# Optimization experiments

Measured on AMD Instinct MI355X. Metric: run time of the kernel, lower is better.

The kernel has to match this reference:

```python
import jax, jax.numpy as jnp
import numpy as np

RANK = 16
ALPHA = 32
SCALING = ALPHA / RANK  # alpha / rank


def setup_inputs() -> dict:
    key = jax.random.key(0)
    k_x, k_w, k_b, k_a, k_bb = jax.random.split(key, 5)
    B, S, D_IN, D_OUT = 4, 2048, 4096, 4096
    x = jax.random.normal(k_x, (B, S, D_IN), dtype=jnp.float32)
    W = jax.random.normal(k_w, (D_OUT, D_IN), dtype=jnp.float32) * (1.0 / np.sqrt(D_IN))
    b = jax.random.normal(k_b, (D_OUT,), dtype=jnp.float32) * 0.02
    # LoRA init: A ~ N(0, 2/rank); B is zeros in the module, but we use small
    # random values so the adapter path is numerically exercised.
    lora_A = jax.random.normal(k_a, (RANK, D_IN), dtype=jnp.float32) * np.sqrt(2.0 / RANK)
    lora_B = jax.random.normal(k_bb, (D_OUT, RANK), dtype=jnp.float32) * 0.02
    return {"x": x, "W": W, "b": b, "lora_A": lora_A, "lora_B": lora_B}


def reference(x, W, b, lora_A, lora_B):
    # Base linear: x @ W^T + b
    base = jnp.einsum("bsd,od->bso", x, W) + b
    # LoRA path, fused as two rank-r matmuls (never materializing B@A):
    # (x @ A^T) @ B^T * scaling  ==  F.linear(x, B@A) * scaling
    xa = jnp.einsum("bsd,rd->bsr", x, lora_A)      # [B,S,r]
    lora = jnp.einsum("bsr,or->bso", xa, lora_B)    # [B,S,D_out]
    return base + lora * SCALING
```

## Files before the change

### kernel.cpp

```cpp
#include <hip/hip_runtime.h>
#include <hip/hip_bf16.h>

#define K_DIM 4096
#define N_DIM 4096
#define R_DIM 16
#define SCALING_F 2.0f

#define BM 256
#define BN 256
#define BK 64

typedef __attribute__((ext_vector_type(8))) short bf16x8;
typedef __attribute__((ext_vector_type(4))) float f32x4;

__device__ __forceinline__ ushort f2bf(float f) {
  union { float f; unsigned u; } v; v.f = f;
  unsigned u = v.u;
  u += 0x7FFF + ((u >> 16) & 1);
  return (ushort)(u >> 16);
}

__global__ __launch_bounds__(256) void prepass_kernel(
    const float* __restrict__ x, ushort* __restrict__ xb,
    const float* __restrict__ W, const float* __restrict__ A,
    const float* __restrict__ Bl, ushort* __restrict__ wb, long n4) {
  if (blockIdx.x < N_DIM) {
    int o = blockIdx.x;
    float breg[R_DIM];
#pragma unroll
    for (int r = 0; r < R_DIM; ++r) breg[r] = Bl[o * R_DIM + r] * SCALING_F;
    for (int d0 = threadIdx.x * 4; d0 < K_DIM; d0 += blockDim.x * 4) {
      float4 w = *(const float4*)(W + (size_t)o * K_DIM + d0);
      float a0 = w.x, a1 = w.y, a2 = w.z, a3 = w.w;
#pragma unroll
      for (int r = 0; r < R_DIM; ++r) {
        float4 a = *(const float4*)(A + (size_t)r * K_DIM + d0);
        a0 += breg[r] * a.x; a1 += breg[r] * a.y;
        a2 += breg[r] * a.z; a3 += breg[r] * a.w;
      }
      ushort4 ob;
      ob.x = f2bf(a0); ob.y = f2bf(a1); ob.z = f2bf(a2); ob.w = f2bf(a3);
      *(ushort4*)(wb + (size_t)o * K_DIM + d0) = ob;
    }
  } else {
    long i = (long)(blockIdx.x - N_DIM) * blockDim.x + threadIdx.x;
    long stride = 2048L * blockDim.x;
    for (; i < n4; i += stride) {
      long idx = i * 4;
      float4 v = *(const float4*)(x + idx);
      ushort4 o;
      o.x = f2bf(v.x); o.y = f2bf(v.y); o.z = f2bf(v.z); o.w = f2bf(v.w);
      *(ushort4*)(xb + idx) = o;
    }
  }
}


#define RS 8192L

#define GLOAD(SRC, LOFF)                                                    \
  __builtin_amdgcn_global_load_lds(                                         \
      (const __attribute__((address_space(1))) void*)(SRC),                 \
      (__attribute__((address_space(3))) void*)(smem + (LOFF)), 16, 0, 0)

#define LDSA(BUF) ((BUF) * 32768)
#define LDSB(BUF) (65536 + (BUF) * 32768)

#define ST_A_EVEN(T, BUF) do {                                              \
    GLOAD(aS + (size_t)(T) * 128,            LDSA(BUF) + ldsDst);           \
    GLOAD(aS + (size_t)(T) * 128 + 128 * RS, LDSA(BUF) + 16384 + ldsDst); } while (0)
#define ST_A_ODD(T, BUF) do {                                               \
    GLOAD(aS + (size_t)(T) * 128 + 64 * RS,  LDSA(BUF) + 8192 + ldsDst);    \
    GLOAD(aS + (size_t)(T) * 128 + 192 * RS, LDSA(BUF) + 24576 + ldsDst); } while (0)
#define ST_B_H0(T, BUF) do {                                                \
    GLOAD(bS + (size_t)(T) * 128,            LDSB(BUF) + ldsDst);           \
    GLOAD(bS + (size_t)(T) * 128 + 64 * RS,  LDSB(BUF) + 8192 + ldsDst); } while (0)
#define ST_B_H1(T, BUF) do {                                                \
    GLOAD(bS + (size_t)(T) * 128 + 128 * RS, LDSB(BUF) + 16384 + ldsDst);   \
    GLOAD(bS + (size_t)(T) * 128 + 192 * RS, LDSB(BUF) + 24576 + ldsDst); } while (0)

#define LDA(M, CK, BUF) (*(const bf16x8*)(smem + LDSA(BUF) + aRd + (M) * 2048 + (CK)))
#define LDB(N, CK, BUF) (*(const bf16x8*)(smem + LDSB(BUF) + bRd + (N) * 2048 + (CK)))

#define PF_A(MB, CK, BUF) do {                                              \
    afr[0] = LDA((MB) + 0, CK, BUF); afr[1] = LDA((MB) + 1, CK, BUF);       \
    afr[2] = LDA((MB) + 2, CK, BUF); afr[3] = LDA((MB) + 3, CK, BUF); } while (0)
#define PF_B_ALL(BUF) do {                                                  \
    bfr[0][0] = LDB(0, cK0, BUF); bfr[0][1] = LDB(0, cK1, BUF);             \
    bfr[1][0] = LDB(1, cK0, BUF); bfr[1][1] = LDB(1, cK1, BUF);             \
    bfr[2][0] = LDB(2, cK0, BUF); bfr[2][1] = LDB(2, cK1, BUF);             \
    bfr[3][0] = LDB(3, cK0, BUF); bfr[3][1] = LDB(3, cK1, BUF); } while (0)

#define MFMA16(MB, KK) do {                                                 \
    _Pragma("unroll") for (int mm = 0; mm < 4; ++mm)                        \
      _Pragma("unroll") for (int nn = 0; nn < 4; ++nn)                      \
        acc[(MB) + mm][nn] = __builtin_amdgcn_mfma_f32_16x16x32_bf16(       \
            afr[mm], bfr[nn][KK], acc[(MB) + mm][nn], 0, 0, 0); } while (0)

#define PH_CORE(MB, KK) do {                                                \
    __builtin_amdgcn_s_barrier();                                           \
    asm volatile("s_waitcnt lgkmcnt(0)");                                   \
    __builtin_amdgcn_s_setprio(1);                                          \
    MFMA16(MB, KK);                                                         \
    __builtin_amdgcn_s_setprio(0); } while (0)

__global__ __launch_bounds__(512, 2) void gemm_lora_kernel(
    const ushort* __restrict__ Ab, const ushort* __restrict__ Bb,
    const float* __restrict__ bias, float* __restrict__ C) {
  __shared__ char smem[131072];

  const int tid = threadIdx.x;
  const int wave = tid >> 6, lane = tid & 63;
  const int wm = wave >> 2, wn = wave & 3;
  const int fr = lane & 15, fq = lane >> 4;

  const int bid = blockIdx.x;
  const int bm = ((bid & 7) << 2) + ((bid >> 3) & 3);
  const int bn = bid >> 5;

  const int trow = tid >> 3;
  const int tswz = ((tid & 7) << 4) ^ ((trow & 7) << 4);
  const char* aS = (const char*)Ab + (size_t)(bm * BM + trow) * RS + tswz;
  const char* bS = (const char*)Bb + (size_t)(bn * BN + trow) * RS + tswz;
  const int ldsDst = tid << 4;

  const int sa  = (fr & 7) << 4;
  const int cK0 = (fq << 4) ^ sa;
  const int cK1 = (64 | (fq << 4)) ^ sa;
  const int aRd = ((wm << 7) + fr) << 7;
  const int bRd = ((wn << 6) + fr) << 7;

  f32x4 acc[8][4];
#pragma unroll
  for (int m = 0; m < 8; ++m)
#pragma unroll
    for (int n = 0; n < 4; ++n) acc[m][n] = (f32x4){0.f, 0.f, 0.f, 0.f};
  bf16x8 afr[4], bfr[4][2];

  ST_B_H0(0, 0); ST_B_H1(0, 0); ST_A_EVEN(0, 0); ST_A_ODD(0, 0);
  ST_B_H0(1, 1); ST_B_H1(1, 1); ST_A_EVEN(1, 1);
  asm volatile("s_waitcnt vmcnt(6)" ::: "memory");
  __builtin_amdgcn_s_barrier();
  PF_B_ALL(0);
  PF_A(0, cK0, 0);

  const int NIT = K_DIM / (2 * BK);
#pragma unroll 1
  for (int i = 0; i < NIT; ++i) {
    const int t1 = 2 * i + 1, t2 = 2 * i + 2, t3 = 2 * i + 3;
    const bool last = (i == NIT - 1);

    ST_A_ODD(t1, 1);
    PH_CORE(0, 0);
    PF_A(0, cK1, 0);
    __builtin_amdgcn_s_barrier();

    if (!last) ST_B_H0(t2, 0);
    PH_CORE(0, 1);
    PF_A(4, cK0, 0);
    __builtin_amdgcn_s_barrier();

    if (!last) ST_B_H1(t2, 0);
    PH_CORE(4, 0);
    PF_A(4, cK1, 0);
    if (last) asm volatile("s_waitcnt vmcnt(0)" ::: "memory");
    else      asm volatile("s_waitcnt vmcnt(4)" ::: "memory");
    __builtin_amdgcn_s_barrier();

    if (!last) ST_A_EVEN(t2, 0);
    PH_CORE(4, 1);
    PF_B_ALL(1);
    PF_A(0, cK0, 1);
    __builtin_amdgcn_s_barrier();

    if (!last) ST_A_ODD(t2, 0);
    PH_CORE(0, 0);
    PF_A(0, cK1, 1);
    __builtin_amdgcn_s_barrier();

    if (!last) ST_B_H0(t3, 1);
    PH_CORE(0, 1);
    PF_A(4, cK0, 1);
    __builtin_amdgcn_s_barrier();

    if (!last) ST_B_H1(t3, 1);
    PH_CORE(4, 0);
    PF_A(4, cK1, 1);
    if (!last) asm volatile("s_waitcnt vmcnt(4)" ::: "memory");
    __builtin_amdgcn_s_barrier();

    if (!last) ST_A_EVEN(t3, 1);
    PH_CORE(4, 1);
    if (!last) {
      PF_B_ALL(0);
      PF_A(0, cK0, 0);
      __builtin_amdgcn_s_barrier();
    }
  }

  const int ccol0 = bn * BN + wn * 64 + fr;
  float bv[4];
#pragma unroll
  for (int n = 0; n < 4; ++n) bv[n] = bias[ccol0 + n * 16];
  const int crow0 = bm * BM + wm * 128 + fq * 4;
#pragma unroll
  for (int m = 0; m < 8; ++m)
#pragma unroll
    for (int n = 0; n < 4; ++n)
#pragma unroll
      for (int v = 0; v < 4; ++v) {
        int row = crow0 + m * 16 + v;
        C[(size_t)row * N_DIM + ccol0 + n * 16] = acc[m][n][v] + bv[n];
      }
}

extern "C" void kernel_launch(void* const* d_in, const int* in_sizes, int n_in,
                              void* d_out, int out_size, void* d_ws, size_t ws_size,
                              hipStream_t stream) {
  const float* x  = (const float*)d_in[0];
  const float* W  = (const float*)d_in[1];
  const float* b  = (const float*)d_in[2];
  const float* lA = (const float*)d_in[3];
  const float* lB = (const float*)d_in[4];
  float* out = (float*)d_out;

  const int M = in_sizes[0] / K_DIM;

  ushort* xb = (ushort*)d_ws;
  ushort* wb = xb + (size_t)M * K_DIM;

  long n4 = (long)M * K_DIM / 4;
  prepass_kernel<<<N_DIM + 2048, 256, 0, stream>>>(x, xb, W, lA, lB, wb, n4);
  gemm_lora_kernel<<<(M / BM) * (N_DIM / BN), 512, 0, stream>>>(xb, wb, b, out);
}
```

Measured before the change: 312.0 us.

## Halve GEMM pipeline phases and reuse LoRA A rows across fold blocks

The GEMM main loop goes from eight barrier phases per two K-tiles to four. Each phase now issues 32 MFMAs over both K halves, with A fragments loaded for both K chunks at once and global-to-LDS stores grouped into larger batches. This cuts barrier and wait overhead, at the cost of more fragment registers and different vmcnt wait points. The weight-folding prepass now handles 8 output rows per block and keeps the 16 LoRA A vectors in registers across those rows, which reduces redundant reads of A.

```diff
diff --git a/kernel.cpp b/kernel.cpp
--- a/kernel.cpp
+++ b/kernel.cpp
@@ -9,6 +9,9 @@
 #define BM 256
 #define BN 256
 #define BK 64
+
+#define FOLD_ROWS 8
+#define FOLD_BLOCKS (N_DIM / FOLD_ROWS)
 
 typedef __attribute__((ext_vector_type(8))) short bf16x8;
 typedef __attribute__((ext_vector_type(4))) float f32x4;
@@ -24,26 +27,33 @@
     const float* __restrict__ x, ushort* __restrict__ xb,
     const float* __restrict__ W, const float* __restrict__ A,
     const float* __restrict__ Bl, ushort* __restrict__ wb, long n4) {
-  if (blockIdx.x < N_DIM) {
-    int o = blockIdx.x;
-    float breg[R_DIM];
-#pragma unroll
-    for (int r = 0; r < R_DIM; ++r) breg[r] = Bl[o * R_DIM + r] * SCALING_F;
-    for (int d0 = threadIdx.x * 4; d0 < K_DIM; d0 += blockDim.x * 4) {
-      float4 w = *(const float4*)(W + (size_t)o * K_DIM + d0);
-      float a0 = w.x, a1 = w.y, a2 = w.z, a3 = w.w;
-#pragma unroll
-      for (int r = 0; r < R_DIM; ++r) {
-        float4 a = *(const float4*)(A + (size_t)r * K_DIM + d0);
-        a0 += breg[r] * a.x; a1 += breg[r] * a.y;
-        a2 += breg[r] * a.z; a3 += breg[r] * a.w;
+  if (blockIdx.x < FOLD_BLOCKS) {
+    const int o0 = blockIdx.x * FOLD_ROWS;
+#pragma unroll 1
+    for (int j = 0; j < 4; ++j) {
+      const int d0 = (threadIdx.x + j * 256) * 4;
+      float4 a[R_DIM];
+#pragma unroll
+      for (int r = 0; r < R_DIM; ++r)
+        a[r] = *(const float4*)(A + (size_t)r * K_DIM + d0);
+#pragma unroll 1
+      for (int rr = 0; rr < FOLD_ROWS; ++rr) {
+        const int o = o0 + rr;
+        float4 w = *(const float4*)(W + (size_t)o * K_DIM + d0);
+        float s0 = w.x, s1 = w.y, s2 = w.z, s3 = w.w;
+#pragma unroll
+        for (int r = 0; r < R_DIM; ++r) {
+          const float bv = Bl[o * R_DIM + r] * SCALING_F;
+          s0 += bv * a[r].x; s1 += bv * a[r].y;
+          s2 += bv * a[r].z; s3 += bv * a[r].w;
+        }
+        ushort4 ob;
+        ob.x = f2bf(s0); ob.y = f2bf(s1); ob.z = f2bf(s2); ob.w = f2bf(s3);
+        *(ushort4*)(wb + (size_t)o * K_DIM + d0) = ob;
       }
-      ushort4 ob;
-      ob.x = f2bf(a0); ob.y = f2bf(a1); ob.z = f2bf(a2); ob.w = f2bf(a3);
-      *(ushort4*)(wb + (size_t)o * K_DIM + d0) = ob;
     }
   } else {
-    long i = (long)(blockIdx.x - N_DIM) * blockDim.x + threadIdx.x;
+    long i = (long)(blockIdx.x - FOLD_BLOCKS) * blockDim.x + threadIdx.x;
     long stride = 2048L * blockDim.x;
     for (; i < n4; i += stride) {
       long idx = i * 4;
@@ -82,27 +92,30 @@
 #define LDA(M, CK, BUF) (*(const bf16x8*)(smem + LDSA(BUF) + aRd + (M) * 2048 + (CK)))
 #define LDB(N, CK, BUF) (*(const bf16x8*)(smem + LDSB(BUF) + bRd + (N) * 2048 + (CK)))
 
-#define PF_A(MB, CK, BUF) do {                                              \
-    afr[0] = LDA((MB) + 0, CK, BUF); afr[1] = LDA((MB) + 1, CK, BUF);       \
-    afr[2] = LDA((MB) + 2, CK, BUF); afr[3] = LDA((MB) + 3, CK, BUF); } while (0)
-#define PF_B_ALL(BUF) do {                                                  \
+#define PF_A8(MB, BUF) do {                                                 \
+    afr[0][0] = LDA((MB) + 0, cK0, BUF); afr[0][1] = LDA((MB) + 0, cK1, BUF); \
+    afr[1][0] = LDA((MB) + 1, cK0, BUF); afr[1][1] = LDA((MB) + 1, cK1, BUF); \
+    afr[2][0] = LDA((MB) + 2, cK0, BUF); afr[2][1] = LDA((MB) + 2, cK1, BUF); \
+    afr[3][0] = LDA((MB) + 3, cK0, BUF); afr[3][1] = LDA((MB) + 3, cK1, BUF); } while (0)
+
+#define PF_B8(BUF) do {                                                     \
     bfr[0][0] = LDB(0, cK0, BUF); bfr[0][1] = LDB(0, cK1, BUF);             \
     bfr[1][0] = LDB(1, cK0, BUF); bfr[1][1] = LDB(1, cK1, BUF);             \
     bfr[2][0] = LDB(2, cK0, BUF); bfr[2][1] = LDB(2, cK1, BUF);             \
     bfr[3][0] = LDB(3, cK0, BUF); bfr[3][1] = LDB(3, cK1, BUF); } while (0)
 
-#define MFMA16(MB, KK) do {                                                 \
+#define MFMA32(MB) do {                                                     \
     _Pragma("unroll") for (int mm = 0; mm < 4; ++mm)                        \
-      _Pragma("unroll") for (int nn = 0; nn < 4; ++nn)                      \
+      _Pragma("unroll") for (int nn = 0; nn < 4; ++nn) {                    \
         acc[(MB) + mm][nn] = __builtin_amdgcn_mfma_f32_16x16x32_bf16(       \
-            afr[mm], bfr[nn][KK], acc[(MB) + mm][nn], 0, 0, 0); } while (0)
-
-#define PH_CORE(MB, KK) do {                                                \
+            afr[mm][0], bfr[nn][0], acc[(MB) + mm][nn], 0, 0, 0);           \
+        acc[(MB) + mm][nn] = __builtin_amdgcn_mfma_f32_16x16x32_bf16(       \
+            afr[mm][1], bfr[nn][1], acc[(MB) + mm][nn], 0, 0, 0); } } while (0)
+
+#define PH_OPEN() do {                                                      \
     __builtin_amdgcn_s_barrier();                                           \
     asm volatile("s_waitcnt lgkmcnt(0)");                                   \
-    __builtin_amdgcn_s_setprio(1);                                          \
-    MFMA16(MB, KK);                                                         \
-    __builtin_amdgcn_s_setprio(0); } while (0)
+    __builtin_amdgcn_s_setprio(1); } while (0)
 
 __global__ __launch_bounds__(512, 2) void gemm_lora_kernel(
     const ushort* __restrict__ Ab, const ushort* __restrict__ Bb,
@@ -135,14 +148,14 @@
   for (int m = 0; m < 8; ++m)
 #pragma unroll
     for (int n = 0; n < 4; ++n) acc[m][n] = (f32x4){0.f, 0.f, 0.f, 0.f};
-  bf16x8 afr[4], bfr[4][2];
+  bf16x8 afr[4][2], bfr[4][2];
 
   ST_B_H0(0, 0); ST_B_H1(0, 0); ST_A_EVEN(0, 0); ST_A_ODD(0, 0);
   ST_B_H0(1, 1); ST_B_H1(1, 1); ST_A_EVEN(1, 1);
   asm volatile("s_waitcnt vmcnt(6)" ::: "memory");
   __builtin_amdgcn_s_barrier();
-  PF_B_ALL(0);
-  PF_A(0, cK0, 0);
+  PF_B8(0);
+  PF_A8(0, 0);
 
   const int NIT = K_DIM / (2 * BK);
 #pragma unroll 1
@@ -151,49 +164,39 @@
     const bool last = (i == NIT - 1);
 
     ST_A_ODD(t1, 1);
-    PH_CORE(0, 0);
-    PF_A(0, cK1, 0);
+    PH_OPEN();
+    MFMA32(0);
+    __builtin_amdgcn_s_setprio(0);
+    PF_A8(4, 0);
+    asm volatile("s_waitcnt vmcnt(2)" ::: "memory");
     __builtin_amdgcn_s_barrier();
 
-    if (!last) ST_B_H0(t2, 0);
-    PH_CORE(0, 1);
-    PF_A(4, cK0, 0);
+    if (!last) { ST_B_H0(t2, 0); ST_B_H1(t2, 0); ST_A_EVEN(t2, 0); }
+    PH_OPEN();
+    MFMA32(4);
+    __builtin_amdgcn_s_setprio(0);
+    PF_B8(1);
+    PF_A8(0, 1);
+    if (last) asm volatile("s_waitcnt vmcnt(0)" ::: "memory");
+    else      asm volatile("s_waitcnt vmcnt(6)" ::: "memory");
     __builtin_amdgcn_s_barrier();
 
-    if (!last) ST_B_H1(t2, 0);
-    PH_CORE(4, 0);
-    PF_A(4, cK1, 0);
-    if (last) asm volatile("s_waitcnt vmcnt(0)" ::: "memory");
-    else      asm volatile("s_waitcnt vmcnt(4)" ::: "memory");
+    if (!last) ST_A_ODD(t2, 0);
+    PH_OPEN();
+    MFMA32(0);
+    __builtin_amdgcn_s_setprio(0);
+    PF_A8(4, 1);
+    if (!last) asm volatile("s_waitcnt vmcnt(2)" ::: "memory");
     __builtin_amdgcn_s_barrier();
 
-    if (!last) ST_A_EVEN(t2, 0);
-    PH_CORE(4, 1);
-    PF_B_ALL(1);
-    PF_A(0, cK0, 1);
-    __builtin_amdgcn_s_barrier();
-
-    if (!last) ST_A_ODD(t2, 0);
-    PH_CORE(0, 0);
-    PF_A(0, cK1, 1);
-    __builtin_amdgcn_s_barrier();
-
-    if (!last) ST_B_H0(t3, 1);
-    PH_CORE(0, 1);
-    PF_A(4, cK0, 1);
-    __builtin_amdgcn_s_barrier();
-
-    if (!last) ST_B_H1(t3, 1);
-    PH_CORE(4, 0);
-    PF_A(4, cK1, 1);
-    if (!last) asm volatile("s_waitcnt vmcnt(4)" ::: "memory");
-    __builtin_amdgcn_s_barrier();
-
-    if (!last) ST_A_EVEN(t3, 1);
-    PH_CORE(4, 1);
+    if (!last) { ST_B_H0(t3, 1); ST_B_H1(t3, 1); ST_A_EVEN(t3, 1); }
+    PH_OPEN();
+    MFMA32(4);
+    __builtin_amdgcn_s_setprio(0);
     if (!last) {
-      PF_B_ALL(0);
-      PF_A(0, cK0, 0);
+      PF_B8(0);
+      PF_A8(0, 0);
+      asm volatile("s_waitcnt vmcnt(6)" ::: "memory");
       __builtin_amdgcn_s_barrier();
     }
   }
@@ -230,6 +233,6 @@
   ushort* wb = xb + (size_t)M * K_DIM;
 
   long n4 = (long)M * K_DIM / 4;
-  prepass_kernel<<<N_DIM + 2048, 256, 0, stream>>>(x, xb, W, lA, lB, wb, n4);
+  prepass_kernel<<<FOLD_BLOCKS + 2048, 256, 0, stream>>>(x, xb, W, lA, lB, wb, n4);
   gemm_lora_kernel<<<(M / BM) * (N_DIM / BN), 512, 0, stream>>>(xb, wb, b, out);
 }
```

Measured after the change: 298.4 us. 4.4% less time.
